# Kernel optimization log

Hardware: AMD Instinct MI355X
Metric: run time of the kernel (lower is better)

Reference implementation:

```python
import jax, jax.numpy as jnp
import numpy as np

N = 100000   # num_embeddings
D = 128      # embedding_dims
E = 128      # edge_output_size
S = 2048     # number of streaming interactions
W_DECAY = 1.0  # Decayer w, decay_method='exp': f(dt) = exp(-w*dt)


def setup_inputs() -> dict:
    key = jax.random.key(0)
    ks = jax.random.split(key, 20)
    def nrm(k, shape, s):
        return jax.random.normal(k, shape, jnp.float32) * s
    sD = 1.0 / np.sqrt(D)
    sE = 1.0 / np.sqrt(E)
    return {
        'heads': jax.random.randint(ks[0], (S,), 0, N, dtype=jnp.int32),
        'tails': jax.random.randint(ks[1], (S,), 0, N, dtype=jnp.int32),
        'times': jnp.sort(jax.random.uniform(ks[2], (S,), jnp.float32) * 100.0),
        # node state tables (nn.Embedding weights in the original)
        'node_rep': nrm(ks[3], (N, D), 0.1),
        'cell_head': nrm(ks[4], (N, D), 0.1),
        'hidden_head': nrm(ks[5], (N, D), 0.1),
        'cell_tail': nrm(ks[6], (N, D), 0.1),
        'hidden_tail': nrm(ks[7], (N, D), 0.1),
        # Edge_updater_nn head / tail: act(rep_h @ W1 + rep_t @ W2 + b)
        'Weh1': nrm(ks[8], (D, E), sD), 'Weh2': nrm(ks[9], (D, E), sD), 'beh': jnp.zeros((E,), jnp.float32),
        'Wet1': nrm(ks[10], (D, E), sD), 'Wet2': nrm(ks[11], (D, E), sD), 'bet': jnp.zeros((E,), jnp.float32),
        # TLSTM head (time-decayed LSTM cell)
        'Wxh': nrm(ks[12], (E, 4 * D), sE), 'Whh': nrm(ks[13], (D, 4 * D), sD), 'bh': jnp.zeros((4 * D,), jnp.float32),
        'Wdh': nrm(ks[14], (D, D), sD), 'bdh': jnp.zeros((D,), jnp.float32),
        # TLSTM tail
        'Wxt': nrm(ks[15], (E, 4 * D), sE), 'Wht': nrm(ks[16], (D, 4 * D), sD), 'bt': jnp.zeros((4 * D,), jnp.float32),
        'Wdt': nrm(ks[17], (D, D), sD), 'bdt': jnp.zeros((D,), jnp.float32),
        # Combiner: tanh(h_head @ Wc1 + h_tail @ Wc2)
        'Wc1': nrm(ks[18], (D, D), sD), 'Wc2': nrm(ks[19], (D, D), sD),
    }


def _tlstm(x, c, h, decay, Wx, Wh, b, Wd, bd):
    # Time-aware LSTM: decompose short-term memory, decay it by elapsed time, recombine.
    cs = jnp.tanh(c @ Wd + bd)      # short-term memory component
    c_adj = c - cs + cs * decay      # adjusted previous cell
    z = x @ Wx + h @ Wh + b          # [4D] gate pre-activations
    i, f, o, g = jnp.split(z, 4)
    i = jax.nn.sigmoid(i); f = jax.nn.sigmoid(f); o = jax.nn.sigmoid(o)
    g = jnp.tanh(g)
    c_new = f * c_adj + i * g
    h_new = o * jnp.tanh(c_new)
    return c_new, h_new


def reference(heads, tails, times, node_rep, cell_head, hidden_head, cell_tail, hidden_tail,
              Weh1, Weh2, beh, Wet1, Wet2, bet,
              Wxh, Whh, bh, Wdh, bdh, Wxt, Wht, bt, Wdt, bdt, Wc1, Wc2):
    recent = jnp.zeros((node_rep.shape[0],), jnp.float32)  # recent_timestamp, init 0

    def step(state, ev):
        rep, ch, hh, ct, ht, rt = state
        h_i, t_i, tm = ev
        rep_h = rep[h_i]                    # gather current reps
        rep_t = rep[t_i]
        dec_h = jnp.exp(-W_DECAY * (tm - rt[h_i]))   # decayer(delta_t)
        dec_t = jnp.exp(-W_DECAY * (tm - rt[t_i]))
        edge_h = jnp.tanh(rep_h @ Weh1 + rep_t @ Weh2 + beh)  # edge_updater_head
        edge_t = jnp.tanh(rep_h @ Wet1 + rep_t @ Wet2 + bet)  # edge_updater_tail
        c_h, h_h = _tlstm(edge_h, ch[h_i], hh[h_i], dec_h, Wxh, Whh, bh, Wdh, bdh)
        c_t, h_t = _tlstm(edge_t, ct[t_i], ht[t_i], dec_t, Wxt, Wht, bt, Wdt, bdt)
        new_rep_h = jnp.tanh(h_h @ Wc1 + ht[h_i] @ Wc2)  # combiner(head hidden, tail hidden)
        new_rep_t = jnp.tanh(hh[t_i] @ Wc1 + h_t @ Wc2)
        # scatter updated state (head written before tail, matching original ordering)
        rep = rep.at[h_i].set(new_rep_h).at[t_i].set(new_rep_t)
        ch = ch.at[h_i].set(c_h); hh = hh.at[h_i].set(h_h)
        ct = ct.at[t_i].set(c_t); ht = ht.at[t_i].set(h_t)
        rt = rt.at[h_i].set(tm).at[t_i].set(tm)
        # if_updated=0: emit pre-update representations for this interaction
        return (rep, ch, hh, ct, ht, rt), (rep_h, rep_t)

    state0 = (node_rep, cell_head, hidden_head, cell_tail, hidden_tail, recent)
    _, (out_h, out_t) = jax.lax.scan(step, state0, (heads, tails, times))
    return jnp.stack([out_h, out_t])  # [2, S, D]
```

## Files before the change

kernel.cpp:

```cpp
#include <hip/hip_runtime.h>
#include <hip/hip_cooperative_groups.h>
#include <math.h>

namespace cg = cooperative_groups;

#define DD 128
#define G 8
#define TPB 512
#define SMAX 2048
#define NBLK_MAX 512

__device__ __forceinline__ float sigmoidf(float x) { return 1.0f / (1.0f + expf(-x)); }

struct PParams {
  const int* heads; const int* tails; const float* times;
  float* node_rep; float* cell_head; float* hidden_head; float* cell_tail; float* hidden_tail;
  const float* beh; const float* bet; const float* bh; const float* bt;
  const float* bdh; const float* bdt;
  const float* Wsrc[12];
  float* Wt[12];
  float* out; float* rt;
  int* order; int* level_off; int* n_levels; int* ph; int* pt;
  int S;
};

__global__ __launch_bounds__(TPB, 4) void process_kernel(PParams p) {
  cg::grid_group grid = cg::this_grid();
  const int tid = threadIdx.x;
  const int bid = (int)blockIdx.x;
  const int nb  = (int)gridDim.x;
  const int Sn  = p.S;
  const int b0  = (bid * 7) & 31;

  __shared__ __align__(16) float S_[16384];
  __shared__ int sIdx[G], hIdx[G], tIdx[G];
  __shared__ float tmv[G], decHs[G], decTs[G];
  __shared__ int sh_changed, sh_maxl;

  const int O_REPH = 0,    O_REPT = 1024, O_CHS = 2048, O_CTS = 3072;
  const int O_ZH   = 0,    O_ZT   = 4096;
  const int O_HHS  = 8192, O_HTS  = 9216, O_HTH = 10240, O_HHT = 11264;
  const int O_EH   = 12288, O_ET  = 13312;
  const int O_CAH  = 14336, O_CAT = 15360;

  {
    const int wv = tid >> 6, lane = tid & 63;
    for (int j = bid * 8 + wv; j < Sn; j += nb * 8) {
      const int myh = p.heads[j], myt = p.tails[j];
      int mph = -1, mpt = -1;
      for (int i = lane; i < j; i += 64) {
        int a = p.heads[i], b = p.tails[i];
        if (a == myh || b == myh) mph = i;
        if (a == myt || b == myt) mpt = i;
      }
#pragma unroll
      for (int off = 32; off > 0; off >>= 1) {
        mph = max(mph, __shfl_down(mph, off));
        mpt = max(mpt, __shfl_down(mpt, off));
      }
      if (lane == 0) { p.ph[j] = mph; p.pt[j] = mpt; }
    }
  }

  {
    for (int i = bid * TPB + tid; i < 98304; i += nb * TPB) {
      int mat, k4, e, E;
      if (i < 32768) {
        mat = i >> 12; int rem = i & 4095; k4 = rem >> 7; e = rem & 127; E = 128;
      } else {
        int i2 = i - 32768; mat = 8 + (i2 >> 14); int rem = i2 & 16383;
        k4 = rem >> 9; e = rem & 511; E = 512;
      }
      const float* Wm = p.Wsrc[mat];
      float4 v;
      v.x = Wm[(4 * k4 + 0) * E + e];
      v.y = Wm[(4 * k4 + 1) * E + e];
      v.z = Wm[(4 * k4 + 2) * E + e];
      v.w = Wm[(4 * k4 + 3) * E + e];
      *(float4*)&p.Wt[mat][(size_t)(k4 * E + e) * 4] = v;
    }
  }
  __threadfence();
  grid.sync();

  if (bid == 0) {
    int* lvl = (int*)S_;
    int* ph2 = lvl + SMAX;
    int* pt2 = ph2 + SMAX;
    int* cnt = pt2 + SMAX;
    for (int j = tid; j < Sn; j += TPB) { ph2[j] = p.ph[j]; pt2[j] = p.pt[j]; lvl[j] = 1; }
    __syncthreads();
    for (int it = 0; it < Sn + 2; ++it) {
      if (tid == 0) sh_changed = 0;
      __syncthreads();
      for (int j = tid; j < Sn; j += TPB) {
        int l = 1;
        int a = ph2[j]; if (a >= 0) l = lvl[a] + 1;
        int b = pt2[j]; if (b >= 0) { int lb = lvl[b] + 1; if (lb > l) l = lb; }
        if (l != lvl[j]) { lvl[j] = l; sh_changed = 1; }
      }
      __syncthreads();
      if (!sh_changed) break;
      __syncthreads();
    }
    if (tid == 0) sh_maxl = 0;
    __syncthreads();
    for (int j = tid; j < Sn; j += TPB) atomicMax(&sh_maxl, lvl[j]);
    __syncthreads();
    const int Mlvl = sh_maxl;
    for (int l = tid; l < Mlvl; l += TPB) cnt[l] = 0;
    __syncthreads();
    for (int j = tid; j < Sn; j += TPB) atomicAdd(&cnt[lvl[j] - 1], 1);
    __syncthreads();
    if (tid == 0) {
      int run = 0; p.level_off[0] = 0;
      for (int l = 0; l < Mlvl; ++l) { run += cnt[l]; p.level_off[l + 1] = run; }
      p.n_levels[0] = Mlvl;
    }
    __syncthreads();
    for (int l = tid; l < Mlvl; l += TPB) cnt[l] = 0;
    __syncthreads();
    for (int j = tid; j < Sn; j += TPB) {
      int lv2 = lvl[j] - 1;
      int pos = p.level_off[lv2] + atomicAdd(&cnt[lv2], 1);
      p.order[pos] = j;
    }
  }
  __threadfence();
  grid.sync();

  int nlv = p.n_levels[0];
  if (nlv < 0) nlv = 0;
  if (nlv > SMAX) nlv = SMAX;

  for (int lv = 0; lv < nlv; ++lv) {
    const int beg = p.level_off[lv], end = p.level_off[lv + 1];

    for (int base = beg + bid * G; base < end; base += nb * G) {
      const int ng = min(G, end - base);
      __syncthreads();
      if (tid < ng) {
        int s = p.order[base + tid]; sIdx[tid] = s;
        int h = p.heads[s], t = p.tails[s];
        hIdx[tid] = h; tIdx[tid] = t;
        float tm = p.times[s]; tmv[tid] = tm;
        decHs[tid] = expf(-(tm - p.rt[h]));
        decTs[tid] = expf(-(tm - p.rt[t]));
      }
      __syncthreads();

      {
        const int d = tid & 127;
        for (int g = tid >> 7; g < ng; g += 4) {
          const size_t oh = (size_t)hIdx[g] * DD + d;
          const size_t ot = (size_t)tIdx[g] * DD + d;
          const int b = d * 8 + g;
          float rh = p.node_rep[oh];
          S_[O_REPH + b] = rh; p.out[(size_t)sIdx[g] * DD + d] = rh;
          S_[O_CHS + b] = p.cell_head[oh];
          S_[O_HHS + b] = p.hidden_head[oh];
          S_[O_HTH + b] = p.hidden_tail[oh];
          float rt_ = p.node_rep[ot];
          S_[O_REPT + b] = rt_; p.out[(size_t)(Sn + sIdx[g]) * DD + d] = rt_;
          S_[O_CTS + b] = p.cell_tail[ot];
          S_[O_HTS + b] = p.hidden_tail[ot];
          S_[O_HHT + b] = p.hidden_head[ot];
        }
      }
      __syncthreads();

      {
        const int role = tid >> 7, e = tid & 127;
        if (role <= 1) {
          const float* W1 = p.Wt[role ? 2 : 0];
          const float* W2 = p.Wt[role ? 3 : 1];
          float bv = role ? p.bet[e] : p.beh[e];
          float a[8];
#pragma unroll
          for (int g = 0; g < 8; ++g) a[g] = bv;
#pragma unroll 4
          for (int k4 = 0; k4 < 32; ++k4) {
            const int kk = (k4 + b0) & 31;
            float4 w1 = *(const float4*)&W1[(kk * 128 + e) * 4];
            float4 w2 = *(const float4*)&W2[(kk * 128 + e) * 4];
            const float* w1f = (const float*)&w1;
            const float* w2f = (const float*)&w2;
#pragma unroll
            for (int jj = 0; jj < 4; ++jj) {
              const int d = (kk << 2) + jj;
              const float wa = w1f[jj], wb = w2f[jj];
              float4 rh0 = *(const float4*)&S_[O_REPH + d * 8];
              float4 rh1 = *(const float4*)&S_[O_REPH + d * 8 + 4];
              float4 rt0 = *(const float4*)&S_[O_REPT + d * 8];
              float4 rt1 = *(const float4*)&S_[O_REPT + d * 8 + 4];
              a[0] += rh0.x * wa + rt0.x * wb; a[1] += rh0.y * wa + rt0.y * wb;
              a[2] += rh0.z * wa + rt0.z * wb; a[3] += rh0.w * wa + rt0.w * wb;
              a[4] += rh1.x * wa + rt1.x * wb; a[5] += rh1.y * wa + rt1.y * wb;
              a[6] += rh1.z * wa + rt1.z * wb; a[7] += rh1.w * wa + rt1.w * wb;
            }
          }
          const int dst = role ? O_ET : O_EH;
          float4 o0, o1;
          o0.x = tanhf(a[0]); o0.y = tanhf(a[1]); o0.z = tanhf(a[2]); o0.w = tanhf(a[3]);
          o1.x = tanhf(a[4]); o1.y = tanhf(a[5]); o1.z = tanhf(a[6]); o1.w = tanhf(a[7]);
          *(float4*)&S_[dst + e * 8] = o0;
          *(float4*)&S_[dst + e * 8 + 4] = o1;
        } else {
          const int th = (role == 2);
          const float* W = p.Wt[th ? 4 : 5];
          const int co = th ? O_CHS : O_CTS;
          float bv = th ? p.bdh[e] : p.bdt[e];
          const float* decA = th ? decHs : decTs;
          float a[8];
#pragma unroll
          for (int g = 0; g < 8; ++g) a[g] = bv;
#pragma unroll 4
          for (int k4 = 0; k4 < 32; ++k4) {
            const int kk = (k4 + b0) & 31;
            float4 wd = *(const float4*)&W[(kk * 128 + e) * 4];
            const float* wdf = (const float*)&wd;
#pragma unroll
            for (int jj = 0; jj < 4; ++jj) {
              const int d = (kk << 2) + jj;
              const float wv = wdf[jj];
              float4 c0 = *(const float4*)&S_[co + d * 8];
              float4 c1 = *(const float4*)&S_[co + d * 8 + 4];
              a[0] += c0.x * wv; a[1] += c0.y * wv; a[2] += c0.z * wv; a[3] += c0.w * wv;
              a[4] += c1.x * wv; a[5] += c1.y * wv; a[6] += c1.z * wv; a[7] += c1.w * wv;
            }
          }
          const int dst = th ? O_CAH : O_CAT;
          float o[8];
#pragma unroll
          for (int g = 0; g < 8; ++g) {
            float cs = tanhf(a[g]);
            float c = S_[co + e * 8 + g];
            o[g] = c - cs + cs * decA[g];
          }
          *(float4*)&S_[dst + e * 8]     = make_float4(o[0], o[1], o[2], o[3]);
          *(float4*)&S_[dst + e * 8 + 4] = make_float4(o[4], o[5], o[6], o[7]);
        }
      }
      __syncthreads();

      {
        const int c = tid;
        const float* TXh = p.Wt[8];  const float* THh = p.Wt[9];
        const float* TXt = p.Wt[10]; const float* THt = p.Wt[11];
        float bhv = p.bh[c], btv = p.bt[c];
        float h[8], t8[8];
#pragma unroll
        for (int g = 0; g < 8; ++g) { h[g] = bhv; t8[g] = btv; }
#pragma unroll 2
        for (int k4 = 0; k4 < 32; ++k4) {
          const int kk = (k4 + b0) & 31;
          float4 wxh = *(const float4*)&TXh[(size_t)(kk * 512 + c) * 4];
          float4 whh = *(const float4*)&THh[(size_t)(kk * 512 + c) * 4];
          float4 wxt = *(const float4*)&TXt[(size_t)(kk * 512 + c) * 4];
          float4 wht = *(const float4*)&THt[(size_t)(kk * 512 + c) * 4];
          const float* fxh = (const float*)&wxh;
          const float* fhh = (const float*)&whh;
          const float* fxt = (const float*)&wxt;
          const float* fht = (const float*)&wht;
#pragma unroll
          for (int jj = 0; jj < 4; ++jj) {
            const int d = (kk << 2) + jj;
            float4 ex0 = *(const float4*)&S_[O_EH + d * 8];
            float4 ex1 = *(const float4*)&S_[O_EH + d * 8 + 4];
            float4 hx0 = *(const float4*)&S_[O_HHS + d * 8];
            float4 hx1 = *(const float4*)&S_[O_HHS + d * 8 + 4];
            float4 et0 = *(const float4*)&S_[O_ET + d * 8];
            float4 et1 = *(const float4*)&S_[O_ET + d * 8 + 4];
            float4 ht0 = *(const float4*)&S_[O_HTS + d * 8];
            float4 ht1 = *(const float4*)&S_[O_HTS + d * 8 + 4];
            const float a1 = fxh[jj], a2 = fhh[jj], a3 = fxt[jj], a4 = fht[jj];
            h[0] += ex0.x * a1 + hx0.x * a2; h[1] += ex0.y * a1 + hx0.y * a2;
            h[2] += ex0.z * a1 + hx0.z * a2; h[3] += ex0.w * a1 + hx0.w * a2;
            h[4] += ex1.x * a1 + hx1.x * a2; h[5] += ex1.y * a1 + hx1.y * a2;
            h[6] += ex1.z * a1 + hx1.z * a2; h[7] += ex1.w * a1 + hx1.w * a2;
            t8[0] += et0.x * a3 + ht0.x * a4; t8[1] += et0.y * a3 + ht0.y * a4;
            t8[2] += et0.z * a3 + ht0.z * a4; t8[3] += et0.w * a3 + ht0.w * a4;
            t8[4] += et1.x * a3 + ht1.x * a4; t8[5] += et1.y * a3 + ht1.y * a4;
            t8[6] += et1.z * a3 + ht1.z * a4; t8[7] += et1.w * a3 + ht1.w * a4;
          }
        }
        *(float4*)&S_[O_ZH + c * 8]     = make_float4(h[0], h[1], h[2], h[3]);
        *(float4*)&S_[O_ZH + c * 8 + 4] = make_float4(h[4], h[5], h[6], h[7]);
        *(float4*)&S_[O_ZT + c * 8]     = make_float4(t8[0], t8[1], t8[2], t8[3]);
        *(float4*)&S_[O_ZT + c * 8 + 4] = make_float4(t8[4], t8[5], t8[6], t8[7]);
      }
      __syncthreads();

      {
        const int side = tid >> 8, sub = (tid >> 7) & 1, e2 = tid & 127;
        const int zo = side ? O_ZT : O_ZH;
        const int co = side ? O_CAT : O_CAH;
        const int no = side ? O_ET : O_EH;
        float* ctab = side ? p.cell_tail : p.cell_head;
        float* htab = side ? p.hidden_tail : p.hidden_head;
        for (int q = 0; q < 4; ++q) {
          int g = sub + 2 * q;
          if (g >= ng) continue;
          float iv = sigmoidf(S_[zo + e2 * 8 + g]);
          float fv = sigmoidf(S_[zo + (128 + e2) * 8 + g]);
          float ov = sigmoidf(S_[zo + (256 + e2) * 8 + g]);
          float gv = tanhf(S_[zo + (384 + e2) * 8 + g]);
          float cadj = S_[co + e2 * 8 + g];
          float cn = fv * cadj + iv * gv;
          float hn = ov * tanhf(cn);
          S_[no + e2 * 8 + g] = hn;
          int node = side ? tIdx[g] : hIdx[g];
          ctab[(size_t)node * DD + e2] = cn;
          htab[(size_t)node * DD + e2] = hn;
        }
        if (tid < 2 * G) {
          int g = tid & (G - 1);
          if (g < ng) p.rt[(tid >= G) ? tIdx[g] : hIdx[g]] = tmv[g];
        }
      }
      __syncthreads();

      {
        const int role = tid >> 7, e = tid & 127;
        if (role <= 1) {
          const int xo = role ? O_HHT : O_EH;
          const int yo = role ? O_ET : O_HTH;
          const float* W1 = p.Wt[6];
          const float* W2 = p.Wt[7];
          float a[8];
#pragma unroll
          for (int g = 0; g < 8; ++g) a[g] = 0.f;
#pragma unroll 4
          for (int k4 = 0; k4 < 32; ++k4) {
            const int kk = (k4 + b0) & 31;
            float4 w1 = *(const float4*)&W1[(kk * 128 + e) * 4];
            float4 w2 = *(const float4*)&W2[(kk * 128 + e) * 4];
            const float* w1f = (const float*)&w1;
            const float* w2f = (const float*)&w2;
#pragma unroll
            for (int jj = 0; jj < 4; ++jj) {
              const int d = (kk << 2) + jj;
              const float wa = w1f[jj], wb = w2f[jj];
              float4 x0 = *(const float4*)&S_[xo + d * 8];
              float4 x1 = *(const float4*)&S_[xo + d * 8 + 4];
              float4 y0 = *(const float4*)&S_[yo + d * 8];
              float4 y1 = *(const float4*)&S_[yo + d * 8 + 4];
              a[0] += x0.x * wa + y0.x * wb; a[1] += x0.y * wa + y0.y * wb;
              a[2] += x0.z * wa + y0.z * wb; a[3] += x0.w * wa + y0.w * wb;
              a[4] += x1.x * wa + y1.x * wb; a[5] += x1.y * wa + y1.y * wb;
              a[6] += x1.z * wa + y1.z * wb; a[7] += x1.w * wa + y1.w * wb;
            }
          }
          if (role == 0) {
#pragma unroll
            for (int g = 0; g < 8; ++g)
              if (g < ng && hIdx[g] != tIdx[g])
                p.node_rep[(size_t)hIdx[g] * DD + e] = tanhf(a[g]);
          } else {
#pragma unroll
            for (int g = 0; g < 8; ++g)
              if (g < ng)
                p.node_rep[(size_t)tIdx[g] * DD + e] = tanhf(a[g]);
          }
        }
      }
    }
    __threadfence();
    grid.sync();
  }
}

extern "C" void kernel_launch(void* const* d_in, const int* in_sizes, int n_in,
                              void* d_out, int out_size, void* d_ws, size_t ws_size,
                              hipStream_t stream) {
  const int* heads = (const int*)d_in[0];
  const int* tails = (const int*)d_in[1];
  const float* times = (const float*)d_in[2];
  float* node_rep    = (float*)d_in[3];
  float* cell_head   = (float*)d_in[4];
  float* hidden_head = (float*)d_in[5];
  float* cell_tail   = (float*)d_in[6];
  float* hidden_tail = (float*)d_in[7];

  const int S = in_sizes[0];
  const int N = in_sizes[3] / DD;

  char* ws = (char*)d_ws;
  size_t off = 0;
  float* rt = (float*)ws;
  off = (((size_t)N * 4) + 511) & ~(size_t)511;
  int* order     = (int*)(ws + off); off += (size_t)SMAX * 4;
  int* level_off = (int*)(ws + off); off += (size_t)(SMAX + 1) * 4;
  int* n_levels  = (int*)(ws + off); off += 64 * 4;
  int* ph        = (int*)(ws + off); off += (size_t)SMAX * 4;
  int* pt        = (int*)(ws + off); off += (size_t)SMAX * 4;
  off = (off + 255) & ~(size_t)255;

  PParams p;
  p.heads = heads; p.tails = tails; p.times = times;
  p.node_rep = node_rep; p.cell_head = cell_head; p.hidden_head = hidden_head;
  p.cell_tail = cell_tail; p.hidden_tail = hidden_tail;
  p.beh = (const float*)d_in[10]; p.bet = (const float*)d_in[13];
  p.bh  = (const float*)d_in[16]; p.bt  = (const float*)d_in[21];
  p.bdh = (const float*)d_in[18]; p.bdt = (const float*)d_in[23];
  p.Wsrc[0] = (const float*)d_in[8];
  p.Wsrc[1] = (const float*)d_in[9];
  p.Wsrc[2] = (const float*)d_in[11];
  p.Wsrc[3] = (const float*)d_in[12];
  p.Wsrc[4] = (const float*)d_in[17];
  p.Wsrc[5] = (const float*)d_in[22];
  p.Wsrc[6] = (const float*)d_in[24];
  p.Wsrc[7] = (const float*)d_in[25];
  p.Wsrc[8] = (const float*)d_in[14];
  p.Wsrc[9] = (const float*)d_in[15];
  p.Wsrc[10] = (const float*)d_in[19];
  p.Wsrc[11] = (const float*)d_in[20];

  for (int m = 0; m < 12; ++m) {
    size_t n = (m < 8) ? 16384 : 65536;
    p.Wt[m] = (float*)(ws + off); off += n * 4;
  }

  p.out = (float*)d_out; p.rt = rt;
  p.order = order; p.level_off = level_off; p.n_levels = n_levels;
  p.ph = ph; p.pt = pt;
  p.S = S;

  hipMemsetAsync(rt, 0, (size_t)N * 4, stream);

  void* args[] = { (void*)&p };

  int dev = 0; hipGetDevice(&dev);
  int nCU = 0;
  hipDeviceGetAttribute(&nCU, hipDeviceAttributeMultiprocessorCount, dev);
  if (nCU <= 0) nCU = 256;
  int maxBlkPerCU = 0;
  if (hipOccupancyMaxActiveBlocksPerMultiprocessor(&maxBlkPerCU, process_kernel, TPB, 0)
      != hipSuccess || maxBlkPerCU < 1)
    maxBlkPerCU = 1;
  long long cap = (long long)nCU * (long long)maxBlkPerCU;
  int grid = (int)(cap < NBLK_MAX ? cap : NBLK_MAX);
  if (grid < 1) grid = nCU;

  hipError_t err = hipLaunchCooperativeKernel(process_kernel, dim3(grid), dim3(TPB),
                                              args, 0, stream);
  if (err != hipSuccess && grid > 256) {
    err = hipLaunchCooperativeKernel(process_kernel, dim3(256), dim3(TPB), args, 0, stream);
    grid = 256;
  }
  if (err != hipSuccess && grid > 128) {
    err = hipLaunchCooperativeKernel(process_kernel, dim3(128), dim3(TPB), args, 0, stream);
    grid = 128;
  }
  if (err != hipSuccess && grid > 64) {
    err = hipLaunchCooperativeKernel(process_kernel, dim3(64), dim3(TPB), args, 0, stream);
  }
}
```

Before: 748.9 us.

## Batch 16 interactions per block with register-prefetched weights and split-K combiner

Each block now processes 16 independent interactions per level instead of 8. Shared-memory buffers double to hold the larger batch, so every weight element loaded from global memory is reused across twice as many rows. Weight float4 loads are software-prefetched one step ahead, and the combiner matmul is split over two K halves using all 512 threads, with the partial sums reduced through shared memory. The grid is capped at 256 blocks with two blocks per CU; in exchange, higher register pressure may cause spills and fewer blocks gives less parallelism on levels with few interactions.

```diff
diff --git a/kernel.cpp b/kernel.cpp
--- a/kernel.cpp
+++ b/kernel.cpp
@@ -5,10 +5,10 @@
 namespace cg = cooperative_groups;
 
 #define DD 128
-#define G 8
+#define G 16
 #define TPB 512
 #define SMAX 2048
-#define NBLK_MAX 512
+#define NBLK_MAX 256
 
 __device__ __forceinline__ float sigmoidf(float x) { return 1.0f / (1.0f + expf(-x)); }
 
@@ -24,24 +24,89 @@
   int S;
 };
 
-__global__ __launch_bounds__(TPB, 4) void process_kernel(PParams p) {
+#define RDP(x0,x1,x2,x3, oo, dd) { const int _b=(oo)+(dd)*16; \
+  x0=*(const float4*)&S_[_b];   x1=*(const float4*)&S_[_b+4]; \
+  x2=*(const float4*)&S_[_b+8]; x3=*(const float4*)&S_[_b+12]; }
+
+#define FMA16_2(wa,wb, x0,x1,x2,x3, y0,y1,y2,y3) { \
+  a[0]+=x0.x*(wa)+y0.x*(wb);  a[1]+=x0.y*(wa)+y0.y*(wb); \
+  a[2]+=x0.z*(wa)+y0.z*(wb);  a[3]+=x0.w*(wa)+y0.w*(wb); \
+  a[4]+=x1.x*(wa)+y1.x*(wb);  a[5]+=x1.y*(wa)+y1.y*(wb); \
+  a[6]+=x1.z*(wa)+y1.z*(wb);  a[7]+=x1.w*(wa)+y1.w*(wb); \
+  a[8]+=x2.x*(wa)+y2.x*(wb);  a[9]+=x2.y*(wa)+y2.y*(wb); \
+  a[10]+=x2.z*(wa)+y2.z*(wb); a[11]+=x2.w*(wa)+y2.w*(wb); \
+  a[12]+=x3.x*(wa)+y3.x*(wb); a[13]+=x3.y*(wa)+y3.y*(wb); \
+  a[14]+=x3.z*(wa)+y3.z*(wb); a[15]+=x3.w*(wa)+y3.w*(wb); }
+
+#define FMA16_1(wa, x0,x1,x2,x3) { \
+  a[0]+=x0.x*(wa);  a[1]+=x0.y*(wa);  a[2]+=x0.z*(wa);  a[3]+=x0.w*(wa); \
+  a[4]+=x1.x*(wa);  a[5]+=x1.y*(wa);  a[6]+=x1.z*(wa);  a[7]+=x1.w*(wa); \
+  a[8]+=x2.x*(wa);  a[9]+=x2.y*(wa);  a[10]+=x2.z*(wa); a[11]+=x2.w*(wa); \
+  a[12]+=x3.x*(wa); a[13]+=x3.y*(wa); a[14]+=x3.z*(wa); a[15]+=x3.w*(wa); }
+
+#define STEP2(oo1,oo2, dd, wa, wb) { float4 _x0,_x1,_x2,_x3,_y0,_y1,_y2,_y3; \
+  RDP(_x0,_x1,_x2,_x3, oo1, dd); RDP(_y0,_y1,_y2,_y3, oo2, dd); \
+  FMA16_2(wa,wb,_x0,_x1,_x2,_x3,_y0,_y1,_y2,_y3); }
+
+#define STEP1(oo, dd, wa) { float4 _x0,_x1,_x2,_x3; \
+  RDP(_x0,_x1,_x2,_x3, oo, dd); FMA16_1(wa,_x0,_x1,_x2,_x3); }
+
+#define K4STEP2(oo1,oo2, kk, wv1, wv2) { const int _d4=(kk)*4; \
+  STEP2(oo1,oo2,_d4+0,(wv1).x,(wv2).x); STEP2(oo1,oo2,_d4+1,(wv1).y,(wv2).y); \
+  STEP2(oo1,oo2,_d4+2,(wv1).z,(wv2).z); STEP2(oo1,oo2,_d4+3,(wv1).w,(wv2).w); }
+
+#define K4STEP1(oo, kk, wv) { const int _d4=(kk)*4; \
+  STEP1(oo,_d4+0,(wv).x); STEP1(oo,_d4+1,(wv).y); \
+  STEP1(oo,_d4+2,(wv).z); STEP1(oo,_d4+3,(wv).w); }
+
+#define BSTEP(dd, c1,c2,c3,c4) { \
+  float4 _e0,_e1,_e2,_e3,_h0,_h1,_h2,_h3,_f0,_f1,_f2,_f3,_q0,_q1,_q2,_q3; \
+  RDP(_e0,_e1,_e2,_e3, O_EH, dd);  RDP(_h0,_h1,_h2,_h3, O_HHS, dd); \
+  RDP(_f0,_f1,_f2,_f3, O_ET, dd);  RDP(_q0,_q1,_q2,_q3, O_HTS, dd); \
+  zh[0]+=_e0.x*(c1)+_h0.x*(c2);  zh[1]+=_e0.y*(c1)+_h0.y*(c2); \
+  zh[2]+=_e0.z*(c1)+_h0.z*(c2);  zh[3]+=_e0.w*(c1)+_h0.w*(c2); \
+  zh[4]+=_e1.x*(c1)+_h1.x*(c2);  zh[5]+=_e1.y*(c1)+_h1.y*(c2); \
+  zh[6]+=_e1.z*(c1)+_h1.z*(c2);  zh[7]+=_e1.w*(c1)+_h1.w*(c2); \
+  zh[8]+=_e2.x*(c1)+_h2.x*(c2);  zh[9]+=_e2.y*(c1)+_h2.y*(c2); \
+  zh[10]+=_e2.z*(c1)+_h2.z*(c2); zh[11]+=_e2.w*(c1)+_h2.w*(c2); \
+  zh[12]+=_e3.x*(c1)+_h3.x*(c2); zh[13]+=_e3.y*(c1)+_h3.y*(c2); \
+  zh[14]+=_e3.z*(c1)+_h3.z*(c2); zh[15]+=_e3.w*(c1)+_h3.w*(c2); \
+  zt[0]+=_f0.x*(c3)+_q0.x*(c4);  zt[1]+=_f0.y*(c3)+_q0.y*(c4); \
+  zt[2]+=_f0.z*(c3)+_q0.z*(c4);  zt[3]+=_f0.w*(c3)+_q0.w*(c4); \
+  zt[4]+=_f1.x*(c3)+_q1.x*(c4);  zt[5]+=_f1.y*(c3)+_q1.y*(c4); \
+  zt[6]+=_f1.z*(c3)+_q1.z*(c4);  zt[7]+=_f1.w*(c3)+_q1.w*(c4); \
+  zt[8]+=_f2.x*(c3)+_q2.x*(c4);  zt[9]+=_f2.y*(c3)+_q2.y*(c4); \
+  zt[10]+=_f2.z*(c3)+_q2.z*(c4); zt[11]+=_f2.w*(c3)+_q2.w*(c4); \
+  zt[12]+=_f3.x*(c3)+_q3.x*(c4); zt[13]+=_f3.y*(c3)+_q3.y*(c4); \
+  zt[14]+=_f3.z*(c3)+_q3.z*(c4); zt[15]+=_f3.w*(c3)+_q3.w*(c4); }
+
+#define K4B(kk, wx1,wh1,wx2,wh2) { const int _d4=(kk)*4; \
+  BSTEP(_d4+0,(wx1).x,(wh1).x,(wx2).x,(wh2).x); \
+  BSTEP(_d4+1,(wx1).y,(wh1).y,(wx2).y,(wh2).y); \
+  BSTEP(_d4+2,(wx1).z,(wh1).z,(wx2).z,(wh2).z); \
+  BSTEP(_d4+3,(wx1).w,(wh1).w,(wx2).w,(wh2).w); }
+
+#define LDW(W,kk)  (*(const float4*)&(W)[(((kk)*128)+e)*4])
+#define LDWB(W,kk) (*(const float4*)&(W)[((size_t)((kk)*512+c))*4])
+
+__global__ __launch_bounds__(TPB, 2) void process_kernel(PParams p) {
   cg::grid_group grid = cg::this_grid();
   const int tid = threadIdx.x;
   const int bid = (int)blockIdx.x;
   const int nb  = (int)gridDim.x;
   const int Sn  = p.S;
-  const int b0  = (bid * 7) & 31;
-
-  __shared__ __align__(16) float S_[16384];
+  const int b0  = ((bid * 8 + (tid >> 6)) * 7) & 31;
+
+  __shared__ __align__(16) float S_[32768];
   __shared__ int sIdx[G], hIdx[G], tIdx[G];
   __shared__ float tmv[G], decHs[G], decTs[G];
   __shared__ int sh_changed, sh_maxl;
 
-  const int O_REPH = 0,    O_REPT = 1024, O_CHS = 2048, O_CTS = 3072;
-  const int O_ZH   = 0,    O_ZT   = 4096;
-  const int O_HHS  = 8192, O_HTS  = 9216, O_HTH = 10240, O_HHT = 11264;
-  const int O_EH   = 12288, O_ET  = 13312;
-  const int O_CAH  = 14336, O_CAT = 15360;
+  const int O_REPH = 0,     O_REPT = 2048,  O_CHS = 4096,  O_CTS = 6144;
+  const int O_ZH   = 0,     O_ZT   = 8192;
+  const int O_HHS  = 16384, O_HTS  = 18432, O_HTH = 20480, O_HHT = 22528;
+  const int O_EH   = 24576, O_ET   = 26624;
+  const int O_CAH  = 28672, O_CAT  = 30720;
 
   {
     const int wv = tid >> 6, lane = tid & 63;
@@ -154,7 +219,7 @@
         for (int g = tid >> 7; g < ng; g += 4) {
           const size_t oh = (size_t)hIdx[g] * DD + d;
           const size_t ot = (size_t)tIdx[g] * DD + d;
-          const int b = d * 8 + g;
+          const int b = d * 16 + g;
           float rh = p.node_rep[oh];
           S_[O_REPH + b] = rh; p.out[(size_t)sIdx[g] * DD + d] = rh;
           S_[O_CHS + b] = p.cell_head[oh];
@@ -175,70 +240,71 @@
           const float* W1 = p.Wt[role ? 2 : 0];
           const float* W2 = p.Wt[role ? 3 : 1];
           float bv = role ? p.bet[e] : p.beh[e];
-          float a[8];
+          float a[16];
 #pragma unroll
-          for (int g = 0; g < 8; ++g) a[g] = bv;
-#pragma unroll 4
-          for (int k4 = 0; k4 < 32; ++k4) {
-            const int kk = (k4 + b0) & 31;
-            float4 w1 = *(const float4*)&W1[(kk * 128 + e) * 4];
-            float4 w2 = *(const float4*)&W2[(kk * 128 + e) * 4];
-            const float* w1f = (const float*)&w1;
-            const float* w2f = (const float*)&w2;
-#pragma unroll
-            for (int jj = 0; jj < 4; ++jj) {
-              const int d = (kk << 2) + jj;
-              const float wa = w1f[jj], wb = w2f[jj];
-              float4 rh0 = *(const float4*)&S_[O_REPH + d * 8];
-              float4 rh1 = *(const float4*)&S_[O_REPH + d * 8 + 4];
-              float4 rt0 = *(const float4*)&S_[O_REPT + d * 8];
-              float4 rt1 = *(const float4*)&S_[O_REPT + d * 8 + 4];
-              a[0] += rh0.x * wa + rt0.x * wb; a[1] += rh0.y * wa + rt0.y * wb;
-              a[2] += rh0.z * wa + rt0.z * wb; a[3] += rh0.w * wa + rt0.w * wb;
-              a[4] += rh1.x * wa + rt1.x * wb; a[5] += rh1.y * wa + rt1.y * wb;
-              a[6] += rh1.z * wa + rt1.z * wb; a[7] += rh1.w * wa + rt1.w * wb;
-            }
+          for (int g = 0; g < 16; ++g) a[g] = bv;
+          float4 wA1 = LDW(W1, b0), wA2 = LDW(W2, b0);
+          const int kB0 = (b0 + 1) & 31;
+          float4 wB1 = LDW(W1, kB0), wB2 = LDW(W2, kB0);
+          for (int k4 = 0; k4 < 32; k4 += 2) {
+            const int kp1 = (k4 + 2 + b0) & 31, kp2 = (k4 + 3 + b0) & 31;
+            float4 nA1 = LDW(W1, kp1), nA2 = LDW(W2, kp1);
+            float4 nB1 = LDW(W1, kp2), nB2 = LDW(W2, kp2);
+            const int kkA = (k4 + b0) & 31, kkB = (k4 + 1 + b0) & 31;
+            K4STEP2(O_REPH, O_REPT, kkA, wA1, wA2);
+            K4STEP2(O_REPH, O_REPT, kkB, wB1, wB2);
+            wA1 = nA1; wA2 = nA2; wB1 = nB1; wB2 = nB2;
           }
           const int dst = role ? O_ET : O_EH;
-          float4 o0, o1;
-          o0.x = tanhf(a[0]); o0.y = tanhf(a[1]); o0.z = tanhf(a[2]); o0.w = tanhf(a[3]);
-          o1.x = tanhf(a[4]); o1.y = tanhf(a[5]); o1.z = tanhf(a[6]); o1.w = tanhf(a[7]);
-          *(float4*)&S_[dst + e * 8] = o0;
-          *(float4*)&S_[dst + e * 8 + 4] = o1;
+          *(float4*)&S_[dst + e*16 + 0]  = make_float4(tanhf(a[0]),  tanhf(a[1]),  tanhf(a[2]),  tanhf(a[3]));
+          *(float4*)&S_[dst + e*16 + 4]  = make_float4(tanhf(a[4]),  tanhf(a[5]),  tanhf(a[6]),  tanhf(a[7]));
+          *(float4*)&S_[dst + e*16 + 8]  = make_float4(tanhf(a[8]),  tanhf(a[9]),  tanhf(a[10]), tanhf(a[11]));
+          *(float4*)&S_[dst + e*16 + 12] = make_float4(tanhf(a[12]), tanhf(a[13]), tanhf(a[14]), tanhf(a[15]));
         } else {
           const int th = (role == 2);
           const float* W = p.Wt[th ? 4 : 5];
           const int co = th ? O_CHS : O_CTS;
           float bv = th ? p.bdh[e] : p.bdt[e];
           const float* decA = th ? decHs : decTs;
-          float a[8];
+          float a[16];
 #pragma unroll
-          for (int g = 0; g < 8; ++g) a[g] = bv;
-#pragma unroll 4
-          for (int k4 = 0; k4 < 32; ++k4) {
-            const int kk = (k4 + b0) & 31;
-            float4 wd = *(const float4*)&W[(kk * 128 + e) * 4];
-            const float* wdf = (const float*)&wd;
-#pragma unroll
-            for (int jj = 0; jj < 4; ++jj) {
-              const int d = (kk << 2) + jj;
-              const float wv = wdf[jj];
-              float4 c0 = *(const float4*)&S_[co + d * 8];
-              float4 c1 = *(const float4*)&S_[co + d * 8 + 4];
-              a[0] += c0.x * wv; a[1] += c0.y * wv; a[2] += c0.z * wv; a[3] += c0.w * wv;
-              a[4] += c1.x * wv; a[5] += c1.y * wv; a[6] += c1.z * wv; a[7] += c1.w * wv;
-            }
+          for (int g = 0; g < 16; ++g) a[g] = bv;
+          float4 wA = LDW(W, b0);
+          float4 wB = LDW(W, (b0 + 1) & 31);
+          for (int k4 = 0; k4 < 32; k4 += 2) {
+            const int kp1 = (k4 + 2 + b0) & 31, kp2 = (k4 + 3 + b0) & 31;
+            float4 nA = LDW(W, kp1);
+            float4 nB = LDW(W, kp2);
+            const int kkA = (k4 + b0) & 31, kkB = (k4 + 1 + b0) & 31;
+            K4STEP1(co, kkA, wA);
+            K4STEP1(co, kkB, wB);
+            wA = nA; wB = nB;
           }
+          float4 c0, c1, c2, c3;
+          RDP(c0, c1, c2, c3, co, e);
           const int dst = th ? O_CAH : O_CAT;
-          float o[8];
-#pragma unroll
-          for (int g = 0; g < 8; ++g) {
-            float cs = tanhf(a[g]);
-            float c = S_[co + e * 8 + g];
-            o[g] = c - cs + cs * decA[g];
-          }
-          *(float4*)&S_[dst + e * 8]     = make_float4(o[0], o[1], o[2], o[3]);
-          *(float4*)&S_[dst + e * 8 + 4] = make_float4(o[4], o[5], o[6], o[7]);
+          float cs;
+          float4 o;
+          cs = tanhf(a[0]);  o.x = c0.x - cs + cs * decA[0];
+          cs = tanhf(a[1]);  o.y = c0.y - cs + cs * decA[1];
+          cs = tanhf(a[2]);  o.z = c0.z - cs + cs * decA[2];
+          cs = tanhf(a[3]);  o.w = c0.w - cs + cs * decA[3];
+          *(float4*)&S_[dst + e*16 + 0] = o;
+          cs = tanhf(a[4]);  o.x = c1.x - cs + cs * decA[4];
+          cs = tanhf(a[5]);  o.y = c1.y - cs + cs * decA[5];
+          cs = tanhf(a[6]);  o.z = c1.z - cs + cs * decA[6];
+          cs = tanhf(a[7]);  o.w = c1.w - cs + cs * decA[7];
+          *(float4*)&S_[dst + e*16 + 4] = o;
+          cs = tanhf(a[8]);  o.x = c2.x - cs + cs * decA[8];
+          cs = tanhf(a[9]);  o.y = c2.y - cs + cs * decA[9];
+          cs = tanhf(a[10]); o.z = c2.z - cs + cs * decA[10];
+          cs = tanhf(a[11]); o.w = c2.w - cs + cs * decA[11];
+          *(float4*)&S_[dst + e*16 + 8] = o;
+          cs = tanhf(a[12]); o.x = c3.x - cs + cs * decA[12];
+          cs = tanhf(a[13]); o.y = c3.y - cs + cs * decA[13];
+          cs = tanhf(a[14]); o.z = c3.z - cs + cs * decA[14];
+          cs = tanhf(a[15]); o.w = c3.w - cs + cs * decA[15];
+          *(float4*)&S_[dst + e*16 + 12] = o;
         }
       }
       __syncthreads();
@@ -247,47 +313,28 @@
         const int c = tid;
         const float* TXh = p.Wt[8];  const float* THh = p.Wt[9];
         const float* TXt = p.Wt[10]; const float* THt = p.Wt[11];
+        float zh[16], zt[16];
         float bhv = p.bh[c], btv = p.bt[c];
-        float h[8], t8[8];
 #pragma unroll
-        for (int g = 0; g < 8; ++g) { h[g] = bhv; t8[g] = btv; }
-#pragma unroll 2
+        for (int g = 0; g < 16; ++g) { zh[g] = bhv; zt[g] = btv; }
+        float4 wxh = LDWB(TXh, b0), whh = LDWB(THh, b0);
+        float4 wxt = LDWB(TXt, b0), wht = LDWB(THt, b0);
         for (int k4 = 0; k4 < 32; ++k4) {
+          const int kkn = (k4 + 1 + b0) & 31;
+          float4 nxh = LDWB(TXh, kkn), nhh = LDWB(THh, kkn);
+          float4 nxt = LDWB(TXt, kkn), nht = LDWB(THt, kkn);
           const int kk = (k4 + b0) & 31;
-          float4 wxh = *(const float4*)&TXh[(size_t)(kk * 512 + c) * 4];
-          float4 whh = *(const float4*)&THh[(size_t)(kk * 512 + c) * 4];
-          float4 wxt = *(const float4*)&TXt[(size_t)(kk * 512 + c) * 4];
-          float4 wht = *(const float4*)&THt[(size_t)(kk * 512 + c) * 4];
-          const float* fxh = (const float*)&wxh;
-          const float* fhh = (const float*)&whh;
-          const float* fxt = (const float*)&wxt;
-          const float* fht = (const float*)&wht;
-#pragma unroll
-          for (int jj = 0; jj < 4; ++jj) {
-            const int d = (kk << 2) + jj;
-            float4 ex0 = *(const float4*)&S_[O_EH + d * 8];
-            float4 ex1 = *(const float4*)&S_[O_EH + d * 8 + 4];
-            float4 hx0 = *(const float4*)&S_[O_HHS + d * 8];
-            float4 hx1 = *(const float4*)&S_[O_HHS + d * 8 + 4];
-            float4 et0 = *(const float4*)&S_[O_ET + d * 8];
-            float4 et1 = *(const float4*)&S_[O_ET + d * 8 + 4];
-            float4 ht0 = *(const float4*)&S_[O_HTS + d * 8];
-            float4 ht1 = *(const float4*)&S_[O_HTS + d * 8 + 4];
-            const float a1 = fxh[jj], a2 = fhh[jj], a3 = fxt[jj], a4 = fht[jj];
-            h[0] += ex0.x * a1 + hx0.x * a2; h[1] += ex0.y * a1 + hx0.y * a2;
-            h[2] += ex0.z * a1 + hx0.z * a2; h[3] += ex0.w * a1 + hx0.w * a2;
-            h[4] += ex1.x * a1 + hx1.x * a2; h[5] += ex1.y * a1 + hx1.y * a2;
-            h[6] += ex1.z * a1 + hx1.z * a2; h[7] += ex1.w * a1 + hx1.w * a2;
-            t8[0] += et0.x * a3 + ht0.x * a4; t8[1] += et0.y * a3 + ht0.y * a4;
-            t8[2] += et0.z * a3 + ht0.z * a4; t8[3] += et0.w * a3 + ht0.w * a4;
-            t8[4] += et1.x * a3 + ht1.x * a4; t8[5] += et1.y * a3 + ht1.y * a4;
-            t8[6] += et1.z * a3 + ht1.z * a4; t8[7] += et1.w * a3 + ht1.w * a4;
-          }
-        }
-        *(float4*)&S_[O_ZH + c * 8]     = make_float4(h[0], h[1], h[2], h[3]);
-        *(float4*)&S_[O_ZH + c * 8 + 4] = make_float4(h[4], h[5], h[6], h[7]);
-        *(float4*)&S_[O_ZT + c * 8]     = make_float4(t8[0], t8[1], t8[2], t8[3]);
-        *(float4*)&S_[O_ZT + c * 8 + 4] = make_float4(t8[4], t8[5], t8[6], t8[7]);
+          K4B(kk, wxh, whh, wxt, wht);
+          wxh = nxh; whh = nhh; wxt = nxt; wht = nht;
+        }
+        *(float4*)&S_[O_ZH + c*16 + 0]  = make_float4(zh[0],  zh[1],  zh[2],  zh[3]);
+        *(float4*)&S_[O_ZH + c*16 + 4]  = make_float4(zh[4],  zh[5],  zh[6],  zh[7]);
+        *(float4*)&S_[O_ZH + c*16 + 8]  = make_float4(zh[8],  zh[9],  zh[10], zh[11]);
+        *(float4*)&S_[O_ZH + c*16 + 12] = make_float4(zh[12], zh[13], zh[14], zh[15]);
+        *(float4*)&S_[O_ZT + c*16 + 0]  = make_float4(zt[0],  zt[1],  zt[2],  zt[3]);
+        *(float4*)&S_[O_ZT + c*16 + 4]  = make_float4(zt[4],  zt[5],  zt[6],  zt[7]);
+        *(float4*)&S_[O_ZT + c*16 + 8]  = make_float4(zt[8],  zt[9],  zt[10], zt[11]);
+        *(float4*)&S_[O_ZT + c*16 + 12] = make_float4(zt[12], zt[13], zt[14], zt[15]);
       }
       __syncthreads();
 
@@ -298,17 +345,17 @@
         const int no = side ? O_ET : O_EH;
         float* ctab = side ? p.cell_tail : p.cell_head;
         float* htab = side ? p.hidden_tail : p.hidden_head;
-        for (int q = 0; q < 4; ++q) {
+        for (int q = 0; q < 8; ++q) {
           int g = sub + 2 * q;
           if (g >= ng) continue;
-          float iv = sigmoidf(S_[zo + e2 * 8 + g]);
-          float fv = sigmoidf(S_[zo + (128 + e2) * 8 + g]);
-          float ov = sigmoidf(S_[zo + (256 + e2) * 8 + g]);
-          float gv = tanhf(S_[zo + (384 + e2) * 8 + g]);
-          float cadj = S_[co + e2 * 8 + g];
+          float iv = sigmoidf(S_[zo + e2 * 16 + g]);
+          float fv = sigmoidf(S_[zo + (128 + e2) * 16 + g]);
+          float ov = sigmoidf(S_[zo + (256 + e2) * 16 + g]);
+          float gv = tanhf(S_[zo + (384 + e2) * 16 + g]);
+          float cadj = S_[co + e2 * 16 + g];
           float cn = fv * cadj + iv * gv;
           float hn = ov * tanhf(cn);
-          S_[no + e2 * 8 + g] = hn;
+          S_[no + e2 * 16 + g] = hn;
           int node = side ? tIdx[g] : hIdx[g];
           ctab[(size_t)node * DD + e2] = cn;
           htab[(size_t)node * DD + e2] = hn;
@@ -321,46 +368,56 @@
       __syncthreads();
 
       {
-        const int role = tid >> 7, e = tid & 127;
-        if (role <= 1) {
-          const int xo = role ? O_HHT : O_EH;
-          const int yo = role ? O_ET : O_HTH;
-          const float* W1 = p.Wt[6];
-          const float* W2 = p.Wt[7];
-          float a[8];
+        const int role = tid >> 8;
+        const int dq = (tid >> 7) & 1;
+        const int e = tid & 127;
+        const int xo = role ? O_HHT : O_EH;
+        const int yo = role ? O_ET  : O_HTH;
+        const float* W1 = p.Wt[6];
+        const float* W2 = p.Wt[7];
+        float a[16];
 #pragma unroll
-          for (int g = 0; g < 8; ++g) a[g] = 0.f;
-#pragma unroll 4
-          for (int k4 = 0; k4 < 32; ++k4) {
-            const int kk = (k4 + b0) & 31;
-            float4 w1 = *(const float4*)&W1[(kk * 128 + e) * 4];
-            float4 w2 = *(const float4*)&W2[(kk * 128 + e) * 4];
-            const float* w1f = (const float*)&w1;
-            const float* w2f = (const float*)&w2;
+        for (int g = 0; g < 16; ++g) a[g] = 0.0f;
+        const int s0 = dq * 16;
+        const int k0 = s0 + (b0 & 15), k1 = s0 + ((b0 + 1) & 15);
+        float4 wA1 = LDW(W1, k0), wA2 = LDW(W2, k0);
+        float4 wB1 = LDW(W1, k1), wB2 = LDW(W2, k1);
+        for (int i = 0; i < 16; i += 2) {
+          const int kp1 = s0 + ((i + 2 + b0) & 15), kp2 = s0 + ((i + 3 + b0) & 15);
+          float4 nA1 = LDW(W1, kp1), nA2 = LDW(W2, kp1);
+          float4 nB1 = LDW(W1, kp2), nB2 = LDW(W2, kp2);
+          const int kkA = s0 + ((i + b0) & 15), kkB = s0 + ((i + 1 + b0) & 15);
+          K4STEP2(xo, yo, kkA, wA1, wA2);
+          K4STEP2(xo, yo, kkB, wB1, wB2);
+          wA1 = nA1; wA2 = nA2; wB1 = nB1; wB2 = nB2;
+        }
+        const int scr = role ? O_CAT : O_CAH;
+        if (dq == 1) {
+          *(float4*)&S_[scr + e*16 + 0]  = make_float4(a[0],  a[1],  a[2],  a[3]);
+          *(float4*)&S_[scr + e*16 + 4]  = make_float4(a[4],  a[5],  a[6],  a[7]);
+          *(float4*)&S_[scr + e*16 + 8]  = make_float4(a[8],  a[9],  a[10], a[11]);
+          *(float4*)&S_[scr + e*16 + 12] = make_float4(a[12], a[13], a[14], a[15]);
+        }
+        __syncthreads();
+        if (dq == 0) {
+          float4 p0 = *(const float4*)&S_[scr + e*16 + 0];
+          float4 p1 = *(const float4*)&S_[scr + e*16 + 4];
+          float4 p2 = *(const float4*)&S_[scr + e*16 + 8];
+          float4 p3 = *(const float4*)&S_[scr + e*16 + 12];
+          a[0] += p0.x;  a[1] += p0.y;  a[2] += p0.z;  a[3] += p0.w;
+          a[4] += p1.x;  a[5] += p1.y;  a[6] += p1.z;  a[7] += p1.w;
+          a[8] += p2.x;  a[9] += p2.y;  a[10] += p2.z; a[11] += p2.w;
+          a[12] += p3.x; a[13] += p3.y; a[14] += p3.z; a[15] += p3.w;
 #pragma unroll
-            for (int jj = 0; jj < 4; ++jj) {
-              const int d = (kk << 2) + jj;
-              const float wa = w1f[jj], wb = w2f[jj];
-              float4 x0 = *(const float4*)&S_[xo + d * 8];
-              float4 x1 = *(const float4*)&S_[xo + d * 8 + 4];
-              float4 y0 = *(const float4*)&S_[yo + d * 8];
-              float4 y1 = *(const float4*)&S_[yo + d * 8 + 4];
-              a[0] += x0.x * wa + y0.x * wb; a[1] += x0.y * wa + y0.y * wb;
-              a[2] += x0.z * wa + y0.z * wb; a[3] += x0.w * wa + y0.w * wb;
-              a[4] += x1.x * wa + y1.x * wb; a[5] += x1.y * wa + y1.y * wb;
-              a[6] += x1.z * wa + y1.z * wb; a[7] += x1.w * wa + y1.w * wb;
+          for (int g = 0; g < 16; ++g) {
+            if (g < ng) {
+              if (role == 0) {
+                if (hIdx[g] != tIdx[g])
+                  p.node_rep[(size_t)hIdx[g] * DD + e] = tanhf(a[g]);
+              } else {
+                p.node_rep[(size_t)tIdx[g] * DD + e] = tanhf(a[g]);
+              }
             }
-          }
-          if (role == 0) {
-#pragma unroll
-            for (int g = 0; g < 8; ++g)
-              if (g < ng && hIdx[g] != tIdx[g])
-                p.node_rep[(size_t)hIdx[g] * DD + e] = tanhf(a[g]);
-          } else {
-#pragma unroll
-            for (int g = 0; g < 8; ++g)
-              if (g < ng)
-                p.node_rep[(size_t)tIdx[g] * DD + e] = tanhf(a[g]);
           }
         }
       }
@@ -444,10 +501,6 @@
 
   hipError_t err = hipLaunchCooperativeKernel(process_kernel, dim3(grid), dim3(TPB),
                                               args, 0, stream);
-  if (err != hipSuccess && grid > 256) {
-    err = hipLaunchCooperativeKernel(process_kernel, dim3(256), dim3(TPB), args, 0, stream);
-    grid = 256;
-  }
   if (err != hipSuccess && grid > 128) {
     err = hipLaunchCooperativeKernel(process_kernel, dim3(128), dim3(TPB), args, 0, stream);
     grid = 128;
```

Result: slower. 827.8 us (+10.5%).
